# Kernel optimization log

Hardware: AMD Instinct MI355X
Metric: run time of the kernel (lower is better)

Reference implementation:

```python
import jax, jax.numpy as jnp
import numpy as np

N_E = 1024
E_DIM = 64
BETA = 0.25
DECAY = 0.99
EPSILON = 1e-5


def setup_inputs() -> dict:
    key = jax.random.key(0)
    k1, k2, k3 = jax.random.split(key, 3)
    z = jax.random.normal(k1, (32, E_DIM, 32, 32), dtype=jnp.float32)
    # codebook initialized uniform(-1/n_e, 1/n_e) as in the torch module
    emb_w = jax.random.uniform(k2, (N_E, E_DIM), minval=-1.0 / N_E, maxval=1.0 / N_E, dtype=jnp.float32)
    ema_cluster_size = jnp.ones((N_E,), dtype=jnp.float32)
    ema_w = jax.random.uniform(k3, (N_E, E_DIM), minval=-1.0 / N_E, maxval=1.0 / N_E, dtype=jnp.float32)
    return {"z": z, "emb_w": emb_w, "ema_cluster_size": ema_cluster_size, "ema_w": ema_w}


def reference(z, emb_w, ema_cluster_size, ema_w):
    B, C, H, W = z.shape  # C == E_DIM
    zf = jnp.transpose(z, (0, 2, 3, 1)).reshape(-1, E_DIM)  # [N, e_dim]
    N = zf.shape[0]

    # squared-distance via ||z||^2 + ||e||^2 - 2 z.e (same expansion as torch code)
    d = (jnp.sum(zf * zf, axis=1, keepdims=True)
         + jnp.sum(emb_w * emb_w, axis=1)
         - 2.0 * zf @ emb_w.T)  # [N, n_e]
    idx = jnp.argmin(d, axis=1)  # [N]

    min_encodings = jax.nn.one_hot(idx, N_E, dtype=jnp.float32)  # [N, n_e]
    # cluster stats via scatter-add (equivalent to one-hot matmuls, cheaper)
    cluster_size = jax.ops.segment_sum(jnp.ones((N,), jnp.float32), idx, num_segments=N_E)
    sum_encodings = jax.ops.segment_sum(zf, idx, num_segments=N_E)  # [n_e, e_dim]

    # EMA update (training path, done before the z_q lookup as in torch)
    new_cs = DECAY * ema_cluster_size + (1.0 - DECAY) * cluster_size
    new_w = DECAY * ema_w + (1.0 - DECAY) * sum_encodings
    n = jnp.sum(new_cs)
    cs_norm = (new_cs + EPSILON) / (n + N_E * EPSILON) * n
    new_emb = new_w / cs_norm[:, None]  # updated codebook

    z_q = new_emb[idx].reshape(B, H, W, C).transpose(0, 3, 1, 2)  # [B,C,H,W]
    loss = BETA * jnp.mean((jax.lax.stop_gradient(z_q) - z) ** 2)
    z_q_st = z + jax.lax.stop_gradient(z_q - z)  # straight-through

    avg_probs = cluster_size / N
    perplexity = jnp.exp(-jnp.sum(avg_probs * jnp.log(avg_probs + 1e-10)))
    return loss, z_q_st, perplexity, min_encodings, idx
```

## Files before the change

### kernel.cpp

```cpp
#include <hip/hip_runtime.h>
#include <math.h>

#define NVEC 32768
#define NE   1024
#define ED   64
#define TOT  2097152
#define NCHUNK 8
#define CHUNK  128
#define MT     64

#define O_LOSS   0
#define O_ZQ     1
#define O_PERP   2097153
#define O_MINENC 2097154
#define O_IDX    35651586

#define W_PIDX   0
#define W_CS     32768
#define W_SUMENC 33792
#define W_NEWEMB 99328
#define W_LOSSP  164864

__global__ void __launch_bounds__(256, 3) k_dist(const float* __restrict__ z,
                                                 const float* __restrict__ emb,
                                                 int* __restrict__ fidx,
                                                 float* __restrict__ out) {
    __shared__ __align__(16) float s_a[64 * 64];
    __shared__ __align__(16) float s_b[64 * 132];
    __shared__ float s_esq[CHUNK];
    __shared__ float s_zsq[MT];

    int tid = threadIdx.x;
    int n0 = blockIdx.x * MT;
    int b = n0 >> 10, hw0 = n0 & 1023;
    const float* zb = z + b * 65536 + hw0;

#pragma unroll
    for (int j = 0; j < 4; ++j) {
        int f4i = j * 256 + tid;
        int c = f4i >> 4, pos = (f4i & 15) * 4;
        float4 v = *(const float4*)(zb + (c << 10) + pos);
        v.x = __fmul_rn(2.0f, v.x);
        v.y = __fmul_rn(2.0f, v.y);
        v.z = __fmul_rn(2.0f, v.z);
        v.w = __fmul_rn(2.0f, v.w);
        *(float4*)(s_a + c * 64 + pos) = v;
    }
    __syncthreads();

    if (tid < MT) {
        float r[8];
#pragma unroll
        for (int j = 0; j < 8; ++j) {
            float v = s_a[j * 64 + tid];
            r[j] = __fmul_rn(v, v);
        }
#pragma unroll
        for (int i = 8; i < 64; i += 8)
#pragma unroll
            for (int j = 0; j < 8; ++j) {
                float v = s_a[(i + j) * 64 + tid];
                r[j] = __fadd_rn(r[j], __fmul_rn(v, v));
            }
        s_zsq[tid] = __fmul_rn(0.25f, __fadd_rn(
            __fadd_rn(__fadd_rn(r[0], r[1]), __fadd_rn(r[2], r[3])),
            __fadd_rn(__fadd_rn(r[4], r[5]), __fadd_rn(r[6], r[7]))));
    }
    __syncthreads();

    int mi = tid & 15, ki = tid >> 4;
    int mbase = mi * 4, kbase = ki * 8;
    float zs[4];
#pragma unroll
    for (int mu = 0; mu < 4; ++mu) zs[mu] = s_zsq[mbase + mu];

    float bd[4];
    int bix[4];
#pragma unroll
    for (int mu = 0; mu < 4; ++mu) { bd[mu] = 3.4e38f; bix[mu] = kbase; }

    for (int q = 0; q < NCHUNK; ++q) {
        int k0 = q * CHUNK;
        __syncthreads();
#pragma unroll
        for (int j = 0; j < 8; ++j) {
            int f4i = j * 256 + tid;
            int kl = f4i >> 4, c4 = f4i & 15;
            float4 v = *(const float4*)(emb + (size_t)(k0 + kl) * ED + c4 * 4);
            int base = ((( kl >> 2) + c4) & 31) * 4 + (kl & 3);
            s_b[(c4 * 4 + 0) * 132 + base] = v.x;
            s_b[(c4 * 4 + 1) * 132 + base] = v.y;
            s_b[(c4 * 4 + 2) * 132 + base] = v.z;
            s_b[(c4 * 4 + 3) * 132 + base] = v.w;
        }
        if (tid < CHUNK) {
            const float* ep = emb + (size_t)(k0 + tid) * ED;
            float r[8];
#pragma unroll
            for (int j = 0; j < 8; ++j) r[j] = __fmul_rn(ep[j], ep[j]);
#pragma unroll
            for (int i = 8; i < 64; i += 8)
#pragma unroll
                for (int j = 0; j < 8; ++j)
                    r[j] = __fadd_rn(r[j], __fmul_rn(ep[i + j], ep[i + j]));
            s_esq[tid] = __fadd_rn(
                __fadd_rn(__fadd_rn(r[0], r[1]), __fadd_rn(r[2], r[3])),
                __fadd_rn(__fadd_rn(r[4], r[5]), __fadd_rn(r[6], r[7])));
        }
        __syncthreads();

        float acc[4][8];
#pragma unroll
        for (int mu = 0; mu < 4; ++mu)
#pragma unroll
            for (int ku = 0; ku < 8; ++ku) acc[mu][ku] = 0.f;

#pragma unroll 4
        for (int c = 0; c < 64; ++c) {
            int c4 = c >> 2;
            float4 av = *(const float4*)(s_a + c * 64 + mbase);
            float4 b0 = *(const float4*)(s_b + c * 132 + ((2 * ki + c4) & 31) * 4);
            float4 b1 = *(const float4*)(s_b + c * 132 + ((2 * ki + 1 + c4) & 31) * 4);
#pragma unroll
            for (int mu = 0; mu < 4; ++mu) {
                float a = (&av.x)[mu];
                acc[mu][0] = __fmaf_rn(a, b0.x, acc[mu][0]);
                acc[mu][1] = __fmaf_rn(a, b0.y, acc[mu][1]);
                acc[mu][2] = __fmaf_rn(a, b0.z, acc[mu][2]);
                acc[mu][3] = __fmaf_rn(a, b0.w, acc[mu][3]);
                acc[mu][4] = __fmaf_rn(a, b1.x, acc[mu][4]);
                acc[mu][5] = __fmaf_rn(a, b1.y, acc[mu][5]);
                acc[mu][6] = __fmaf_rn(a, b1.z, acc[mu][6]);
                acc[mu][7] = __fmaf_rn(a, b1.w, acc[mu][7]);
            }
        }

#pragma unroll
        for (int mu = 0; mu < 4; ++mu)
#pragma unroll
            for (int ku = 0; ku < 8; ++ku) {
                float d = __fsub_rn(__fadd_rn(zs[mu], s_esq[kbase + ku]),
                                    acc[mu][ku]);
                if (d < bd[mu]) { bd[mu] = d; bix[mu] = k0 + kbase + ku; }
            }
    }

    __syncthreads();
    float* red_d = s_b;
    int* red_i = (int*)(s_b + 1024);
#pragma unroll
    for (int mu = 0; mu < 4; ++mu) {
        red_d[ki * 64 + mbase + mu] = bd[mu];
        red_i[ki * 64 + mbase + mu] = bix[mu];
    }
    __syncthreads();
    if (tid < MT) {
        float best = red_d[tid];
        int bi = red_i[tid];
#pragma unroll
        for (int q = 1; q < 16; ++q) {
            float d = red_d[q * 64 + tid];
            int i = red_i[q * 64 + tid];
            if (d < best || (d == best && i < bi)) { best = d; bi = i; }
        }
        fidx[n0 + tid] = bi;
        out[O_IDX + n0 + tid] = (float)bi;
    }
}

__global__ void __launch_bounds__(256) k_sumenc(const int* __restrict__ idx,
                                                const float* __restrict__ z,
                                                float* __restrict__ cs,
                                                float* __restrict__ sumenc) {
    int k = blockIdx.x;
    int wave = threadIdx.x >> 6, lane = threadIdx.x & 63;
    float acc = 0.f;
    int cnt = 0;
    int base = wave * 8192;
    for (int it = 0; it < 128; ++it) {
        int n0 = base + it * 64;
        int idv = idx[n0 + lane];
        unsigned long long m = __ballot(idv == k);
        cnt += __popcll(m);
        while (m) {
            int bit = __ffsll((unsigned long long)m) - 1;
            m &= m - 1;
            int n = n0 + bit;
            int b = n >> 10, hw = n & 1023;
            acc = __fadd_rn(acc, z[b * 65536 + lane * 1024 + hw]);
        }
    }
    __shared__ float sacc[4][64];
    __shared__ int scnt[4];
    sacc[wave][lane] = acc;
    if (lane == 0) scnt[wave] = cnt;
    __syncthreads();
    if (wave == 0) {
        float t = __fadd_rn(__fadd_rn(sacc[0][lane], sacc[1][lane]),
                            __fadd_rn(sacc[2][lane], sacc[3][lane]));
        sumenc[k * ED + lane] = t;
        if (lane == 0) cs[k] = (float)(scnt[0] + scnt[1] + scnt[2] + scnt[3]);
    }
}

__global__ void __launch_bounds__(1024) k_ema(const float* __restrict__ ema_cs,
                                              const float* __restrict__ ema_w,
                                              const float* __restrict__ cs,
                                              const float* __restrict__ sumenc,
                                              float* __restrict__ newemb,
                                              float* __restrict__ out) {
    int k = threadIdx.x;
    float c = cs[k];
    float ncs = 0.99f * ema_cs[k] + (1.0f - 0.99f) * c;
    float p = c * (1.0f / (float)NVEC);
    float e = p * logf(p + 1e-10f);
    float rn_ = ncs, re_ = e;
#pragma unroll
    for (int o = 32; o > 0; o >>= 1) {
        rn_ += __shfl_down(rn_, o, 64);
        re_ += __shfl_down(re_, o, 64);
    }
    __shared__ float sn[16], se_[16];
    __shared__ float s_n;
    int wave = k >> 6, lane = k & 63;
    if (lane == 0) { sn[wave] = rn_; se_[wave] = re_; }
    __syncthreads();
    if (k == 0) {
        float tn = 0.f, te = 0.f;
#pragma unroll
        for (int w = 0; w < 16; ++w) { tn += sn[w]; te += se_[w]; }
        s_n = tn;
        out[O_PERP] = expf(-te);
    }
    __syncthreads();
    float nt = s_n;
    float csn = (ncs + 1e-5f) / (nt + 1024.0f * 1e-5f) * nt;
    __shared__ float s_csn[NE];
    s_csn[k] = csn;
    __syncthreads();
    for (int t = k; t < NE * ED; t += 1024) {
        float nw = 0.99f * ema_w[t] + (1.0f - 0.99f) * sumenc[t];
        newemb[t] = nw / s_csn[t >> 6];
    }
}

__global__ void __launch_bounds__(256) k_zq(const float* __restrict__ z,
                                            const int* __restrict__ idx,
                                            const float* __restrict__ newemb,
                                            float* __restrict__ out,
                                            float* __restrict__ lossp) {
    __shared__ int sbi[16];
    if (threadIdx.x < 16) sbi[threadIdx.x] = idx[blockIdx.x * 16 + threadIdx.x];
    __syncthreads();

    float local = 0.f;
#pragma unroll
    for (int i = 0; i < 4; ++i) {
        int t = blockIdx.x * 256 + threadIdx.x + i * 524288;
        int b = t >> 16, c = (t >> 10) & 63, hw = t & 1023;
        int n = (b << 10) | hw;
        float e = newemb[idx[n] * ED + c];
        float zv = z[t];
        float diff = e - zv;
        out[O_ZQ + t] = zv + diff;
        local = fmaf(diff, diff, local);
    }

    int t = threadIdx.x;
    int r0 = blockIdx.x * 16;
    for (int r = 0; r < 16; ++r) {
        int rbi = sbi[r];
        float* rp = out + O_MINENC + (size_t)(r0 + r) * NE;
        if (t < 254) {
            int col = 2 + t * 4;
            float4 v;
            v.x = (col == rbi) ? 1.0f : 0.0f;
            v.y = (col + 1 == rbi) ? 1.0f : 0.0f;
            v.z = (col + 2 == rbi) ? 1.0f : 0.0f;
            v.w = (col + 3 == rbi) ? 1.0f : 0.0f;
            *(float4*)(rp + col) = v;
        } else if (t == 254) {
            float2 v;
            v.x = (0 == rbi) ? 1.0f : 0.0f;
            v.y = (1 == rbi) ? 1.0f : 0.0f;
            *(float2*)(rp) = v;
        } else {
            float4 v;
            v.x = (1018 == rbi) ? 1.0f : 0.0f;
            v.y = (1019 == rbi) ? 1.0f : 0.0f;
            v.z = (1020 == rbi) ? 1.0f : 0.0f;
            v.w = (1021 == rbi) ? 1.0f : 0.0f;
            *(float4*)(rp + 1018) = v;
            float2 w;
            w.x = (1022 == rbi) ? 1.0f : 0.0f;
            w.y = (1023 == rbi) ? 1.0f : 0.0f;
            *(float2*)(rp + 1022) = w;
        }
    }

#pragma unroll
    for (int o = 32; o > 0; o >>= 1) local += __shfl_down(local, o, 64);
    __shared__ float sp[4];
    int wave = threadIdx.x >> 6;
    if ((threadIdx.x & 63) == 0) sp[wave] = local;
    __syncthreads();
    if (threadIdx.x == 0)
        lossp[blockIdx.x] = (sp[0] + sp[1]) + (sp[2] + sp[3]);
}

__global__ void __launch_bounds__(256) k_fin(const float* __restrict__ lossp,
                                             float* __restrict__ out) {
    float v = 0.f;
#pragma unroll
    for (int i = 0; i < 8; ++i) v += lossp[i * 256 + threadIdx.x];
#pragma unroll
    for (int o = 32; o > 0; o >>= 1) v += __shfl_down(v, o, 64);
    __shared__ float sp[4];
    int wave = threadIdx.x >> 6;
    if ((threadIdx.x & 63) == 0) sp[wave] = v;
    __syncthreads();
    if (threadIdx.x == 0)
        out[O_LOSS] = 0.25f * (((sp[0] + sp[1]) + (sp[2] + sp[3])) * (1.0f / (float)TOT));
}

extern "C" void kernel_launch(void* const* d_in, const int* in_sizes, int n_in,
                              void* d_out, int out_size, void* d_ws, size_t ws_size,
                              hipStream_t stream) {
    const float* z      = (const float*)d_in[0];
    const float* emb    = (const float*)d_in[1];
    const float* ema_cs = (const float*)d_in[2];
    const float* ema_w  = (const float*)d_in[3];
    float* out = (float*)d_out;
    float* ws  = (float*)d_ws;

    k_dist<<<512, 256, 0, stream>>>(z, emb, (int*)(ws + W_PIDX), out);
    k_sumenc<<<NE, 256, 0, stream>>>((const int*)(ws + W_PIDX), z, ws + W_CS,
                                     ws + W_SUMENC);
    k_ema<<<1, 1024, 0, stream>>>(ema_cs, ema_w, ws + W_CS, ws + W_SUMENC,
                                  ws + W_NEWEMB, out);
    k_zq<<<2048, 256, 0, stream>>>(z, (const int*)(ws + W_PIDX), ws + W_NEWEMB, out,
                                   ws + W_LOSSP);
    k_fin<<<1, 256, 0, stream>>>(ws + W_LOSSP, out);
}
```

Before: 286.0 us.

## Fuse cluster stats into distance kernel via atomics and precompute codebook norms

Removes the k_sumenc kernel, which scanned all indices once per code, and instead accumulates counts and per-code sums with atomics at the end of k_dist, reusing the z tile already in shared memory. Codebook squared norms are computed once in a new k_pre kernel instead of redundantly in every k_dist block; k_pre also zeroes the accumulators. The loss is reduced with a float atomic, removing the k_fin launch. Float atomics make the summation order nondeterministic, and hot codes can cause atomic contention.

```diff
diff --git a/kernel.cpp b/kernel.cpp
--- a/kernel.cpp
+++ b/kernel.cpp
@@ -19,16 +19,47 @@
 #define W_CS     32768
 #define W_SUMENC 33792
 #define W_NEWEMB 99328
-#define W_LOSSP  164864
+#define W_ESQ    164864
+
+
+__global__ void __launch_bounds__(256) k_pre(const float* __restrict__ emb,
+                                             float* __restrict__ ws,
+                                             float* __restrict__ out) {
+    int b = blockIdx.x;
+    if (b < 65) {
+        int i = b * 256 + threadIdx.x;
+        float4 zv; zv.x = 0.f; zv.y = 0.f; zv.z = 0.f; zv.w = 0.f;
+        *(float4*)(ws + W_CS + i * 4) = zv;
+        if (b == 0 && threadIdx.x == 0) out[O_LOSS] = 0.f;
+    } else {
+        int code = (b - 65) * 256 + threadIdx.x;
+        const float* ep = emb + (size_t)code * ED;
+        float r[8];
+#pragma unroll
+        for (int j = 0; j < 8; ++j) r[j] = __fmul_rn(ep[j], ep[j]);
+#pragma unroll
+        for (int i = 8; i < 64; i += 8)
+#pragma unroll
+            for (int j = 0; j < 8; ++j)
+                r[j] = __fadd_rn(r[j], __fmul_rn(ep[i + j], ep[i + j]));
+        ws[W_ESQ + code] = __fadd_rn(
+            __fadd_rn(__fadd_rn(r[0], r[1]), __fadd_rn(r[2], r[3])),
+            __fadd_rn(__fadd_rn(r[4], r[5]), __fadd_rn(r[6], r[7])));
+    }
+}
 
 __global__ void __launch_bounds__(256, 3) k_dist(const float* __restrict__ z,
                                                  const float* __restrict__ emb,
+                                                 const float* __restrict__ esq_g,
                                                  int* __restrict__ fidx,
+                                                 int* __restrict__ cnt,
+                                                 float* __restrict__ sumenc,
                                                  float* __restrict__ out) {
     __shared__ __align__(16) float s_a[64 * 64];
     __shared__ __align__(16) float s_b[64 * 132];
     __shared__ float s_esq[CHUNK];
     __shared__ float s_zsq[MT];
+    __shared__ int s_bi[MT];
 
     int tid = threadIdx.x;
     int n0 = blockIdx.x * MT;
@@ -93,20 +124,7 @@
             s_b[(c4 * 4 + 2) * 132 + base] = v.z;
             s_b[(c4 * 4 + 3) * 132 + base] = v.w;
         }
-        if (tid < CHUNK) {
-            const float* ep = emb + (size_t)(k0 + tid) * ED;
-            float r[8];
-#pragma unroll
-            for (int j = 0; j < 8; ++j) r[j] = __fmul_rn(ep[j], ep[j]);
-#pragma unroll
-            for (int i = 8; i < 64; i += 8)
-#pragma unroll
-                for (int j = 0; j < 8; ++j)
-                    r[j] = __fadd_rn(r[j], __fmul_rn(ep[i + j], ep[i + j]));
-            s_esq[tid] = __fadd_rn(
-                __fadd_rn(__fadd_rn(r[0], r[1]), __fadd_rn(r[2], r[3])),
-                __fadd_rn(__fadd_rn(r[4], r[5]), __fadd_rn(r[6], r[7])));
-        }
+        if (tid < CHUNK) s_esq[tid] = esq_g[k0 + tid];
         __syncthreads();
 
         float acc[4][8];
@@ -165,52 +183,32 @@
         }
         fidx[n0 + tid] = bi;
         out[O_IDX + n0 + tid] = (float)bi;
-    }
-}
-
-__global__ void __launch_bounds__(256) k_sumenc(const int* __restrict__ idx,
-                                                const float* __restrict__ z,
-                                                float* __restrict__ cs,
-                                                float* __restrict__ sumenc) {
-    int k = blockIdx.x;
-    int wave = threadIdx.x >> 6, lane = threadIdx.x & 63;
-    float acc = 0.f;
-    int cnt = 0;
-    int base = wave * 8192;
-    for (int it = 0; it < 128; ++it) {
-        int n0 = base + it * 64;
-        int idv = idx[n0 + lane];
-        unsigned long long m = __ballot(idv == k);
-        cnt += __popcll(m);
-        while (m) {
-            int bit = __ffsll((unsigned long long)m) - 1;
-            m &= m - 1;
-            int n = n0 + bit;
-            int b = n >> 10, hw = n & 1023;
-            acc = __fadd_rn(acc, z[b * 65536 + lane * 1024 + hw]);
-        }
-    }
-    __shared__ float sacc[4][64];
-    __shared__ int scnt[4];
-    sacc[wave][lane] = acc;
-    if (lane == 0) scnt[wave] = cnt;
-    __syncthreads();
-    if (wave == 0) {
-        float t = __fadd_rn(__fadd_rn(sacc[0][lane], sacc[1][lane]),
-                            __fadd_rn(sacc[2][lane], sacc[3][lane]));
-        sumenc[k * ED + lane] = t;
-        if (lane == 0) cs[k] = (float)(scnt[0] + scnt[1] + scnt[2] + scnt[3]);
+        s_bi[tid] = bi;
+        atomicAdd(&cnt[bi], 1);
+    }
+    __syncthreads();
+
+    {
+        int lane = tid & 63, w = tid >> 6;
+        int myb = s_bi[lane];
+        float* se = sumenc + ((size_t)myb << 6);
+#pragma unroll
+        for (int i = 0; i < 16; ++i) {
+            int c = (w << 4) | i;
+            float v = __fmul_rn(0.5f, s_a[(c << 6) + lane]);
+            unsafeAtomicAdd(se + c, v);
+        }
     }
 }
 
 __global__ void __launch_bounds__(1024) k_ema(const float* __restrict__ ema_cs,
                                               const float* __restrict__ ema_w,
-                                              const float* __restrict__ cs,
+                                              const int* __restrict__ cnt,
                                               const float* __restrict__ sumenc,
                                               float* __restrict__ newemb,
                                               float* __restrict__ out) {
     int k = threadIdx.x;
-    float c = cs[k];
+    float c = (float)cnt[k];
     float ncs = 0.99f * ema_cs[k] + (1.0f - 0.99f) * c;
     float p = c * (1.0f / (float)NVEC);
     float e = p * logf(p + 1e-10f);
@@ -247,8 +245,7 @@
 __global__ void __launch_bounds__(256) k_zq(const float* __restrict__ z,
                                             const int* __restrict__ idx,
                                             const float* __restrict__ newemb,
-                                            float* __restrict__ out,
-                                            float* __restrict__ lossp) {
+                                            float* __restrict__ out) {
     __shared__ int sbi[16];
     if (threadIdx.x < 16) sbi[threadIdx.x] = idx[blockIdx.x * 16 + threadIdx.x];
     __syncthreads();
@@ -305,22 +302,8 @@
     if ((threadIdx.x & 63) == 0) sp[wave] = local;
     __syncthreads();
     if (threadIdx.x == 0)
-        lossp[blockIdx.x] = (sp[0] + sp[1]) + (sp[2] + sp[3]);
-}
-
-__global__ void __launch_bounds__(256) k_fin(const float* __restrict__ lossp,
-                                             float* __restrict__ out) {
-    float v = 0.f;
-#pragma unroll
-    for (int i = 0; i < 8; ++i) v += lossp[i * 256 + threadIdx.x];
-#pragma unroll
-    for (int o = 32; o > 0; o >>= 1) v += __shfl_down(v, o, 64);
-    __shared__ float sp[4];
-    int wave = threadIdx.x >> 6;
-    if ((threadIdx.x & 63) == 0) sp[wave] = v;
-    __syncthreads();
-    if (threadIdx.x == 0)
-        out[O_LOSS] = 0.25f * (((sp[0] + sp[1]) + (sp[2] + sp[3])) * (1.0f / (float)TOT));
+        unsafeAtomicAdd(out + O_LOSS,
+                        ((sp[0] + sp[1]) + (sp[2] + sp[3])) * (0.25f / (float)TOT));
 }
 
 extern "C" void kernel_launch(void* const* d_in, const int* in_sizes, int n_in,
@@ -333,12 +316,11 @@
     float* out = (float*)d_out;
     float* ws  = (float*)d_ws;
 
-    k_dist<<<512, 256, 0, stream>>>(z, emb, (int*)(ws + W_PIDX), out);
-    k_sumenc<<<NE, 256, 0, stream>>>((const int*)(ws + W_PIDX), z, ws + W_CS,
-                                     ws + W_SUMENC);
-    k_ema<<<1, 1024, 0, stream>>>(ema_cs, ema_w, ws + W_CS, ws + W_SUMENC,
-                                  ws + W_NEWEMB, out);
-    k_zq<<<2048, 256, 0, stream>>>(z, (const int*)(ws + W_PIDX), ws + W_NEWEMB, out,
-                                   ws + W_LOSSP);
-    k_fin<<<1, 256, 0, stream>>>(ws + W_LOSSP, out);
-}
+    k_pre<<<69, 256, 0, stream>>>(emb, ws, out);
+    k_dist<<<512, 256, 0, stream>>>(z, emb, ws + W_ESQ, (int*)(ws + W_PIDX),
+                                    (int*)(ws + W_CS), ws + W_SUMENC, out);
+    k_ema<<<1, 1024, 0, stream>>>(ema_cs, ema_w, (const int*)(ws + W_CS),
+                                  ws + W_SUMENC, ws + W_NEWEMB, out);
+    k_zq<<<2048, 256, 0, stream>>>(z, (const int*)(ws + W_PIDX), ws + W_NEWEMB,
+                                   out);
+}
```

Measured after the change: 404.7 us. 41.5% more time.
